# Performance work log

Measured on AMD Instinct MI355X. Metric: run time of the kernel, lower is better.

Reference implementation:

```python
import jax, jax.numpy as jnp
import numpy as np

B, C, E = 64, 32, 4
D_MODEL, PRED_LEN = 1024, 720
L_LIST = [32, 16, 8, 4]  # seq_len=512 / patch_sizes [16,32,64,128]
EPS = float(np.finfo(float).eps)


def setup_inputs() -> dict:
    key = jax.random.key(0)
    ks = jax.random.split(key, 16)
    inp = {}
    for i, L in enumerate(L_LIST):
        inp[f"xs{i}"] = jax.random.normal(ks[i], (B, C, L, D_MODEL), dtype=jnp.float32)
    inp["gates"] = jax.random.uniform(ks[4], (B, E), dtype=jnp.float32)
    w_scale = 1.0 / np.sqrt(D_MODEL)
    for i in range(E):
        inp[f"W{i}"] = jax.random.normal(ks[5 + i], (D_MODEL, PRED_LEN), dtype=jnp.float32) * w_scale
        inp[f"b{i}"] = jax.random.normal(ks[9 + i], (PRED_LEN,), dtype=jnp.float32) * 0.01
    return inp


def reference(xs0, xs1, xs2, xs3, gates, W0, b0, W1, b1, W2, b2, W3, b3):
    xs = [xs0, xs1, xs2, xs3]
    Ws = [W0, W1, W2, W3]
    bs = [b0, b1, b2, b3]
    # per-expert linear on last token: [B,C,D] @ [D,P] + [P] -> [B,C,P]
    outs = jnp.stack(
        [jnp.einsum("bcd,dp->bcp", x[:, :, -1, :], W) + b for x, W, b in zip(xs, Ws, bs)]
    )  # [E,B,C,P]
    # dense-gate combine(): sum_e gates[b,e] * exp(out_e[b])
    combined = jnp.einsum("ebcp,be->bcp", jnp.exp(outs), gates)  # [B,C,P]
    combined = jnp.where(combined == 0, EPS, combined)
    out = jnp.log(combined)  # [B,C,P]
    return out.transpose(0, 2, 1)  # 'B C P -> B P C'
```

## Files before the change

kernel.cpp:

```cpp
#include <hip/hip_runtime.h>
#include <hip/hip_bf16.h>


typedef __attribute__((ext_vector_type(4))) float f32x4;
typedef __attribute__((ext_vector_type(8))) short bf16x8;
typedef __attribute__((ext_vector_type(4))) unsigned short u16x4;
typedef __attribute__((ext_vector_type(8))) unsigned short u16x8;

#define EPSV 2.2204460492503131e-16f

__device__ __forceinline__ unsigned short f2bf(float f) {
  unsigned u = __builtin_bit_cast(unsigned, f);
  u += 0x7fffu + ((u >> 16) & 1u);
  return (unsigned short)(u >> 16);
}
__device__ __forceinline__ float bf2f(unsigned short h) {
  unsigned u = ((unsigned)h) << 16;
  return __builtin_bit_cast(float, u);
}

__device__ __forceinline__ void gload_lds16(const void* g, void* l) {
  __builtin_amdgcn_global_load_lds(
      (const __attribute__((address_space(1))) unsigned int*)g,
      (__attribute__((address_space(3))) unsigned int*)l, 16, 0, 0);
}

__global__ __launch_bounds__(256) void prep_fused(
    const float* __restrict__ xs0, const float* __restrict__ xs1,
    const float* __restrict__ xs2, const float* __restrict__ xs3,
    const float* __restrict__ W0, const float* __restrict__ W1,
    const float* __restrict__ W2, const float* __restrict__ W3,
    unsigned short* __restrict__ Xb, unsigned short* __restrict__ Wb)
{
  __shared__ __align__(16) unsigned short tile[64 * 72];
  const int tid = threadIdx.x;
  if (blockIdx.x < 4096) {
    const int i = blockIdx.x * 256 + tid;
    const int e = i >> 18;
    const int rem = i & 262143;
    const int m = rem >> 7;
    const int kc = rem & 127;
    const float* xp = (e == 0) ? xs0 : (e == 1) ? xs1 : (e == 2) ? xs2 : xs3;
    const int L = 32 >> e;
    const float* src = xp + ((size_t)m * L + (L - 1)) * 1024 + kc * 8;
    f32x4 v0 = *(const f32x4*)src;
    f32x4 v1 = *(const f32x4*)(src + 4);
    u16x8 pk;
    pk[0] = f2bf(v0[0]); pk[1] = f2bf(v0[1]); pk[2] = f2bf(v0[2]); pk[3] = f2bf(v0[3]);
    pk[4] = f2bf(v1[0]); pk[5] = f2bf(v1[1]); pk[6] = f2bf(v1[2]); pk[7] = f2bf(v1[3]);
    *(u16x8*)(Xb + ((size_t)e * 2048 + m) * 1024 + kc * 8) = pk;
  } else {
    const int wI = blockIdx.x - 4096;
    const int k0 = (wI & 15) * 64;
    const int rest = wI >> 4;
    const int nb = (rest % 12) * 64;
    const int e = rest / 12;
    const float* Wp = (e == 0) ? W0 : (e == 1) ? W1 : (e == 2) ? W2 : W3;
    const int n_c = tid & 15;
    const int r = tid >> 4;
    const int n0 = nb + n_c * 4;
#pragma unroll
    for (int j = 0; j < 4; ++j) {
      const int row = r + j * 16;
      f32x4 v = {0.f, 0.f, 0.f, 0.f};
      if (n0 < 720) v = *(const f32x4*)(Wp + (size_t)(k0 + row) * 720 + n0);
#pragma unroll
      for (int d = 0; d < 4; ++d) tile[(n_c * 4 + d) * 72 + row] = f2bf(v[d]);
    }
    __syncthreads();
    const int n_l = tid >> 2;
    const int kq = tid & 3;
    if (nb + n_l < 720) {
#pragma unroll
      for (int q = 0; q < 2; ++q) {
        const int chunk = q * 4 + kq;
        *(u16x8*)(Wb + ((size_t)e * 720 + nb + n_l) * 1024 + k0 + chunk * 8) =
            *(const u16x8*)(tile + n_l * 72 + chunk * 8);
      }
    }
  }
}

__global__ __launch_bounds__(256) void moe_gemm_e(
    const unsigned short* __restrict__ Xb, const unsigned short* __restrict__ Wb,
    const float* __restrict__ gates,
    const float* __restrict__ b0, const float* __restrict__ b1,
    const float* __restrict__ b2, const float* __restrict__ b3,
    unsigned short* __restrict__ planes)
{
  __shared__ __align__(16) unsigned char smem[49152];
  unsigned short* a_lds = (unsigned short*)smem;
  unsigned short* b_lds = (unsigned short*)(smem + 32768);

  const int tid = threadIdx.x;
  const int lane = tid & 63;
  const int wid = tid >> 6;
  const int wm = wid >> 1, wn = wid & 1;

  const int id = ((int)blockIdx.x & 7) * 96 + ((int)blockIdx.x >> 3);
  const int nt = id % 12;
  const int mt = (id / 12) % 16;
  const int e  = id / 192;
  const int nbase = nt * 64;

  const float* barr[4] = {b0, b1, b2, b3};
  float g_r[2];
#pragma unroll
  for (int h = 0; h < 2; ++h)
    g_r[h] = gates[(mt * 4 + wm * 2 + h) * 4 + e];
  float bias_r[2];
#pragma unroll
  for (int nf = 0; nf < 2; ++nf) {
    int col = nbase + wn * 32 + nf * 16 + (lane & 15);
    bias_r[nf] = barr[e][col < 720 ? col : 719];
  }

  const unsigned short* asrc = Xb + (size_t)e * 2048 * 1024 + (size_t)mt * 128 * 1024;
  const unsigned short* bsrc = Wb + (size_t)e * 720 * 1024;

  auto stage = [&](int k0, int buf) {
#pragma unroll
    for (int j = 0; j < 4; ++j) {
      const int C = j * 256 + tid;
      const int row = C >> 3, c = C & 7;
      gload_lds16(asrc + (size_t)row * 1024 + k0 + ((c ^ (row & 7)) * 8),
                  a_lds + buf * 8192 + C * 8);
    }
#pragma unroll
    for (int j = 0; j < 2; ++j) {
      const int C = j * 256 + tid;
      const int row = C >> 3, c = C & 7;
      int n = nbase + row; if (n > 719) n = 719;
      gload_lds16(bsrc + (size_t)n * 1024 + k0 + ((c ^ (row & 7)) * 8),
                  b_lds + buf * 4096 + C * 8);
    }
  };

  auto compute = [&](int buf, f32x4 (&acc)[4][2]) {
    const unsigned short* al = a_lds + buf * 8192;
    const unsigned short* bl = b_lds + buf * 4096;
#pragma unroll
    for (int ks = 0; ks < 2; ++ks) {
      const int kb = ks * 64 + (lane >> 4) * 16;
      bf16x8 af[4], bfm[2];
#pragma unroll
      for (int mf = 0; mf < 4; ++mf) {
        const int r = wm * 64 + mf * 16 + (lane & 15);
        const int byte = (r * 128 + kb) ^ ((r & 7) << 4);
        af[mf] = *(const bf16x8*)((const char*)al + byte);
      }
#pragma unroll
      for (int nf = 0; nf < 2; ++nf) {
        const int r = wn * 32 + nf * 16 + (lane & 15);
        const int byte = (r * 128 + kb) ^ ((r & 7) << 4);
        bfm[nf] = *(const bf16x8*)((const char*)bl + byte);
      }
#pragma unroll
      for (int mf = 0; mf < 4; ++mf)
#pragma unroll
        for (int nf = 0; nf < 2; ++nf)
          acc[mf][nf] = __builtin_amdgcn_mfma_f32_16x16x32_bf16(
              af[mf], bfm[nf], acc[mf][nf], 0, 0, 0);
    }
  };

  f32x4 acc[4][2] = {};
  int cur = 0;
  stage(0, 0);
  __syncthreads();
  for (int kt = 0; kt < 16; ++kt) {
    if (kt < 15) stage((kt + 1) * 64, cur ^ 1);
    compute(cur, acc);
    __syncthreads();
    cur ^= 1;
  }

#pragma unroll
  for (int nf = 0; nf < 2; ++nf) {
    const int p = nbase + wn * 32 + nf * 16 + (lane & 15);
    if (p < 720) {
#pragma unroll
      for (int mf = 0; mf < 4; ++mf) {
        const int m0 = mt * 128 + wm * 64 + mf * 16 + ((lane >> 4) << 2);
        const float g = g_r[mf >> 1];
        unsigned short* dst = planes + ((size_t)e * 2048 + m0) * 720 + p;
#pragma unroll
        for (int j = 0; j < 4; ++j)
          dst[j * 720] = f2bf(g * __expf(acc[mf][nf][j] + bias_r[nf]));
      }
    }
  }
}

__global__ __launch_bounds__(256) void reduce_log(
    const unsigned short* __restrict__ planes, float* __restrict__ out)
{
  __shared__ __align__(16) float t[64 * 36];
  const int nt = blockIdx.x;
  const int b  = blockIdx.y;
  const int nbase = nt * 64;
  const int tid = threadIdx.x;

  {
    const int row = tid >> 3;
    const int pc = tid & 7;
    int p0 = nbase + pc * 8;
    if (p0 > 712) p0 = 712;
    const size_t base = ((size_t)b * 32 + row) * 720 + p0;
    float s[8] = {};
#pragma unroll
    for (int pl = 0; pl < 4; ++pl) {
      u16x8 v = *(const u16x8*)(planes + (size_t)pl * 2048 * 720 + base);
#pragma unroll
      for (int d = 0; d < 8; ++d) s[d] += bf2f(v[d]);
    }
    const int pbase_l = (p0 - nbase);
#pragma unroll
    for (int d = 0; d < 8; ++d) {
      float v = s[d];
      v = (v == 0.0f) ? EPSV : v;
      t[(pbase_l + d) * 36 + row] = __logf(v);
    }
  }
  __syncthreads();
#pragma unroll
  for (int it = 0; it < 2; ++it) {
    const int i = it * 256 + tid;
    const int p_l = i >> 3;
    const int cc = i & 7;
    const int p = nbase + p_l;
    if (p < 720) {
      f32x4 v = *(const f32x4*)(t + p_l * 36 + cc * 4);
      *(f32x4*)(out + ((size_t)b * 720 + p) * 32 + cc * 4) = v;
    }
  }
}

__global__ __launch_bounds__(256) void moe_head_fallback(
    const float* __restrict__ xs0, const float* __restrict__ xs1,
    const float* __restrict__ xs2, const float* __restrict__ xs3,
    const float* __restrict__ gates,
    const float* __restrict__ W0, const float* __restrict__ b0,
    const float* __restrict__ W1, const float* __restrict__ b1,
    const float* __restrict__ W2, const float* __restrict__ b2,
    const float* __restrict__ W3, const float* __restrict__ b3,
    float* __restrict__ out)
{
  __shared__ __align__(16) unsigned short a_lds[64 * 64];
  __shared__ __align__(16) unsigned short b_lds[64 * 64];
  __shared__ __align__(16) float t_lds[4][32 * 36];
  const int tid = threadIdx.x;
  const int lane = tid & 63;
  const int wid = tid >> 6;
  const int wm = wid >> 1, wn = wid & 1;
  const int nt = blockIdx.x, mt = blockIdx.y;
  const int mbase = mt * 64, nbase = nt * 64;
  const float* xarr[4] = {xs0, xs1, xs2, xs3};
  const float* Warr[4] = {W0, W1, W2, W3};
  const float* barr[4] = {b0, b1, b2, b3};
  constexpr int Larr[4] = {32, 16, 8, 4};
  f32x4 comb[2][2] = {};
#pragma unroll
  for (int e = 0; e < 4; ++e) {
    const int L = Larr[e];
    const float* xlast = xarr[e] + (size_t)(L - 1) * 1024;
    const size_t xstride = (size_t)L * 1024;
    const float* Wp = Warr[e];
    f32x4 acc[2][2] = {};
    for (int kt = 0; kt < 16; ++kt) {
      const int k0 = kt * 64;
      __syncthreads();
      {
        const int k_l = (tid & 15) * 4;
        const int r0 = tid >> 4;
#pragma unroll
        for (int j = 0; j < 4; ++j) {
          const int row = r0 + j * 16;
          f32x4 v = *(const f32x4*)(xlast + (size_t)(mbase + row) * xstride + (k0 + k_l));
          u16x4 pk;
          pk[0] = f2bf(v[0]); pk[1] = f2bf(v[1]); pk[2] = f2bf(v[2]); pk[3] = f2bf(v[3]);
          const int byte = (row * 128 + k_l * 2) ^ ((row & 7) << 4);
          *(u16x4*)((char*)a_lds + byte) = pk;
        }
      }
      {
        const int n_l = tid & 63;
        const int kq = tid >> 6;
        const int n_g = nbase + n_l;
        const bool nok = (n_g < 720);
        const float* wcol = Wp + n_g;
#pragma unroll
        for (int g = 0; g < 4; ++g) {
          const int k_l = kq * 4 + g * 16;
          float w0 = 0.f, w1 = 0.f, w2 = 0.f, w3 = 0.f;
          if (nok) {
            const float* s = wcol + (size_t)(k0 + k_l) * 720;
            w0 = s[0]; w1 = s[720]; w2 = s[1440]; w3 = s[2160];
          }
          u16x4 pk;
          pk[0] = f2bf(w0); pk[1] = f2bf(w1); pk[2] = f2bf(w2); pk[3] = f2bf(w3);
          const int byte = (n_l * 128 + k_l * 2) ^ ((n_l & 7) << 4);
          *(u16x4*)((char*)b_lds + byte) = pk;
        }
      }
      __syncthreads();
#pragma unroll
      for (int ks = 0; ks < 2; ++ks) {
        const int kb2 = (ks * 32 + (lane >> 4) * 8) * 2;
        bf16x8 af[2], bfr[2];
#pragma unroll
        for (int mf = 0; mf < 2; ++mf) {
          const int r = wm * 32 + mf * 16 + (lane & 15);
          const int byte = (r * 128 + kb2) ^ ((r & 7) << 4);
          af[mf] = *(const bf16x8*)((const char*)a_lds + byte);
        }
#pragma unroll
        for (int nf = 0; nf < 2; ++nf) {
          const int r = wn * 32 + nf * 16 + (lane & 15);
          const int byte = (r * 128 + kb2) ^ ((r & 7) << 4);
          bfr[nf] = *(const bf16x8*)((const char*)b_lds + byte);
        }
#pragma unroll
        for (int mf = 0; mf < 2; ++mf)
#pragma unroll
          for (int nf = 0; nf < 2; ++nf)
            acc[mf][nf] = __builtin_amdgcn_mfma_f32_16x16x32_bf16(
                af[mf], bfr[nf], acc[mf][nf], 0, 0, 0);
      }
    }
    {
      const int b_idx = mt * 2 + wm;
      const float g = gates[b_idx * 4 + e];
#pragma unroll
      for (int nf = 0; nf < 2; ++nf) {
        const int col = nbase + wn * 32 + nf * 16 + (lane & 15);
        const float bias = (col < 720) ? barr[e][col] : 0.0f;
#pragma unroll
        for (int mf = 0; mf < 2; ++mf)
#pragma unroll
          for (int j = 0; j < 4; ++j)
            comb[mf][nf][j] += g * __expf(acc[mf][nf][j] + bias);
      }
    }
  }
  {
    float* tl = &t_lds[wid][0];
#pragma unroll
    for (int mf = 0; mf < 2; ++mf)
#pragma unroll
      for (int nf = 0; nf < 2; ++nf)
#pragma unroll
        for (int j = 0; j < 4; ++j) {
          const int row_l = mf * 16 + (lane >> 4) * 4 + j;
          const int col_l = nf * 16 + (lane & 15);
          float v = comb[mf][nf][j];
          v = (v == 0.0f) ? EPSV : v;
          tl[col_l * 36 + row_l] = __logf(v);
        }
    __syncthreads();
    const int b_idx = mt * 2 + wm;
    const int pbase = nbase + wn * 32;
#pragma unroll
    for (int it = 0; it < 4; ++it) {
      const int p_l = it * 8 + (lane >> 3);
      const int p = pbase + p_l;
      if (p < 720) {
        f32x4 v = *(const f32x4*)(tl + p_l * 36 + (lane & 7) * 4);
        *(f32x4*)(out + ((size_t)b_idx * 720 + p) * 32 + (lane & 7) * 4) = v;
      }
    }
  }
}

extern "C" void kernel_launch(void* const* d_in, const int* in_sizes, int n_in,
                              void* d_out, int out_size, void* d_ws, size_t ws_size,
                              hipStream_t stream) {
  const size_t xb_elems = (size_t)4 * 2048 * 1024;
  const size_t wb_elems = (size_t)4 * 720 * 1024;
  const size_t plane_elems = (size_t)4 * 2048 * 720;
  const size_t need = (xb_elems + wb_elems + plane_elems) * 2;
  if (ws_size >= need) {
    unsigned short* Xb = (unsigned short*)d_ws;
    unsigned short* Wb = Xb + xb_elems;
    unsigned short* planes = Wb + wb_elems;
    prep_fused<<<4096 + 768, 256, 0, stream>>>(
        (const float*)d_in[0], (const float*)d_in[1],
        (const float*)d_in[2], (const float*)d_in[3],
        (const float*)d_in[5], (const float*)d_in[7],
        (const float*)d_in[9], (const float*)d_in[11],
        Xb, Wb);
    moe_gemm_e<<<768, 256, 0, stream>>>(
        Xb, Wb, (const float*)d_in[4],
        (const float*)d_in[6], (const float*)d_in[8],
        (const float*)d_in[10], (const float*)d_in[12],
        planes);
    reduce_log<<<dim3(12, 64), 256, 0, stream>>>(planes, (float*)d_out);
  } else {
    moe_head_fallback<<<dim3(12, 32), 256, 0, stream>>>(
        (const float*)d_in[0], (const float*)d_in[1],
        (const float*)d_in[2], (const float*)d_in[3],
        (const float*)d_in[4],
        (const float*)d_in[5], (const float*)d_in[6],
        (const float*)d_in[7], (const float*)d_in[8],
        (const float*)d_in[9], (const float*)d_in[10],
        (const float*)d_in[11], (const float*)d_in[12],
        (float*)d_out);
  }
}
```

Before: 39.71 us.

## Pre-swizzle operands into MFMA fragment layout and load directly to registers

The prep kernel now writes X and W in bf16 laid out in the exact per-lane MFMA fragment order. The GEMM can then drop LDS staging, double buffering and barriers and read fragments straight from global memory with coalesced 16-byte loads. The GEMM block shrinks to 2 waves, each computing a 64x64 tile with a 4x4 accumulator grid. This removes LDS traffic and sync overhead, but gives up cross-wave reuse through shared memory. Each W fragment is now read from global or L2 by more waves, and memory latency is hidden only by occupancy and the 2x unroll.

After: 56.28 us. +41.7%, slower.

```diff
diff --git a/kernel.cpp b/kernel.cpp
--- a/kernel.cpp
+++ b/kernel.cpp
@@ -19,18 +19,13 @@
   return __builtin_bit_cast(float, u);
 }
 
-__device__ __forceinline__ void gload_lds16(const void* g, void* l) {
-  __builtin_amdgcn_global_load_lds(
-      (const __attribute__((address_space(1))) unsigned int*)g,
-      (__attribute__((address_space(3))) unsigned int*)l, 16, 0, 0);
-}
 
 __global__ __launch_bounds__(256) void prep_fused(
     const float* __restrict__ xs0, const float* __restrict__ xs1,
     const float* __restrict__ xs2, const float* __restrict__ xs3,
     const float* __restrict__ W0, const float* __restrict__ W1,
     const float* __restrict__ W2, const float* __restrict__ W3,
-    unsigned short* __restrict__ Xb, unsigned short* __restrict__ Wb)
+    unsigned short* __restrict__ Xf, unsigned short* __restrict__ Wf)
 {
   __shared__ __align__(16) unsigned short tile[64 * 72];
   const int tid = threadIdx.x;
@@ -48,7 +43,12 @@
     u16x8 pk;
     pk[0] = f2bf(v0[0]); pk[1] = f2bf(v0[1]); pk[2] = f2bf(v0[2]); pk[3] = f2bf(v0[3]);
     pk[4] = f2bf(v1[0]); pk[5] = f2bf(v1[1]); pk[6] = f2bf(v1[2]); pk[7] = f2bf(v1[3]);
-    *(u16x8*)(Xb + ((size_t)e * 2048 + m) * 1024 + kc * 8) = pk;
+    const int mp = m >> 6, mf = (m >> 4) & 3, ml = m & 15;
+    const int kt = kc >> 3, ks = (kc >> 2) & 1, kl = kc & 3;
+    const int lane = kl * 16 + ml;
+    const size_t dst = ((size_t)(((((e * 32 + mp) * 16 + kt) * 2 + ks) * 4 + mf)) * 512)
+                       + lane * 8;
+    *(u16x8*)(Xf + dst) = pk;
   } else {
     const int wI = blockIdx.x - 4096;
     const int k0 = (wI & 15) * 64;
@@ -70,123 +70,78 @@
     __syncthreads();
     const int n_l = tid >> 2;
     const int kq = tid & 3;
-    if (nb + n_l < 720) {
-#pragma unroll
-      for (int q = 0; q < 2; ++q) {
-        const int chunk = q * 4 + kq;
-        *(u16x8*)(Wb + ((size_t)e * 720 + nb + n_l) * 1024 + k0 + chunk * 8) =
-            *(const u16x8*)(tile + n_l * 72 + chunk * 8);
-      }
-    }
-  }
-}
-
-__global__ __launch_bounds__(256) void moe_gemm_e(
-    const unsigned short* __restrict__ Xb, const unsigned short* __restrict__ Wb,
+    const int np = nb >> 6;
+    const int kt = k0 >> 6;
+    const int nf = (n_l >> 4) & 3, nl = n_l & 15;
+#pragma unroll
+    for (int q = 0; q < 2; ++q) {
+      const int chunk = q * 4 + kq;
+      const int ks = chunk >> 2, kl = chunk & 3;
+      const size_t dst = ((size_t)(((((e * 12 + np) * 16 + kt) * 2 + ks) * 4 + nf)) * 512)
+                         + (kl * 16 + nl) * 8;
+      *(u16x8*)(Wf + dst) = *(const u16x8*)(tile + n_l * 72 + chunk * 8);
+    }
+  }
+}
+
+__global__ __launch_bounds__(128) void moe_gemm_frag(
+    const unsigned short* __restrict__ Xf, const unsigned short* __restrict__ Wf,
     const float* __restrict__ gates,
     const float* __restrict__ b0, const float* __restrict__ b1,
     const float* __restrict__ b2, const float* __restrict__ b3,
     unsigned short* __restrict__ planes)
 {
-  __shared__ __align__(16) unsigned char smem[49152];
-  unsigned short* a_lds = (unsigned short*)smem;
-  unsigned short* b_lds = (unsigned short*)(smem + 32768);
-
   const int tid = threadIdx.x;
   const int lane = tid & 63;
-  const int wid = tid >> 6;
-  const int wm = wid >> 1, wn = wid & 1;
+  const int wm = tid >> 6;
 
   const int id = ((int)blockIdx.x & 7) * 96 + ((int)blockIdx.x >> 3);
-  const int nt = id % 12;
-  const int mt = (id / 12) % 16;
-  const int e  = id / 192;
-  const int nbase = nt * 64;
+  const int np  = id % 12;
+  const int mtB = (id / 12) & 15;
+  const int e   = id / 192;
+  const int mp  = mtB * 2 + wm;
+
+  const unsigned short* A = Xf + (size_t)(e * 32 + mp) * 65536 + (size_t)lane * 8;
+  const unsigned short* B = Wf + (size_t)(e * 12 + np) * 65536 + (size_t)lane * 8;
+
+  f32x4 acc[4][4] = {};
+#pragma unroll 2
+  for (int kt = 0; kt < 16; ++kt) {
+#pragma unroll
+    for (int ks = 0; ks < 2; ++ks) {
+      const int off = kt * 4096 + ks * 2048;
+      bf16x8 af[4], bf[4];
+#pragma unroll
+      for (int mf = 0; mf < 4; ++mf) af[mf] = *(const bf16x8*)(A + off + mf * 512);
+#pragma unroll
+      for (int nf = 0; nf < 4; ++nf) bf[nf] = *(const bf16x8*)(B + off + nf * 512);
+#pragma unroll
+      for (int mf = 0; mf < 4; ++mf)
+#pragma unroll
+        for (int nf = 0; nf < 4; ++nf)
+          acc[mf][nf] = __builtin_amdgcn_mfma_f32_16x16x32_bf16(
+              af[mf], bf[nf], acc[mf][nf], 0, 0, 0);
+    }
+  }
 
   const float* barr[4] = {b0, b1, b2, b3};
   float g_r[2];
 #pragma unroll
   for (int h = 0; h < 2; ++h)
-    g_r[h] = gates[(mt * 4 + wm * 2 + h) * 4 + e];
-  float bias_r[2];
-#pragma unroll
-  for (int nf = 0; nf < 2; ++nf) {
-    int col = nbase + wn * 32 + nf * 16 + (lane & 15);
-    bias_r[nf] = barr[e][col < 720 ? col : 719];
-  }
-
-  const unsigned short* asrc = Xb + (size_t)e * 2048 * 1024 + (size_t)mt * 128 * 1024;
-  const unsigned short* bsrc = Wb + (size_t)e * 720 * 1024;
-
-  auto stage = [&](int k0, int buf) {
-#pragma unroll
-    for (int j = 0; j < 4; ++j) {
-      const int C = j * 256 + tid;
-      const int row = C >> 3, c = C & 7;
-      gload_lds16(asrc + (size_t)row * 1024 + k0 + ((c ^ (row & 7)) * 8),
-                  a_lds + buf * 8192 + C * 8);
-    }
-#pragma unroll
-    for (int j = 0; j < 2; ++j) {
-      const int C = j * 256 + tid;
-      const int row = C >> 3, c = C & 7;
-      int n = nbase + row; if (n > 719) n = 719;
-      gload_lds16(bsrc + (size_t)n * 1024 + k0 + ((c ^ (row & 7)) * 8),
-                  b_lds + buf * 4096 + C * 8);
-    }
-  };
-
-  auto compute = [&](int buf, f32x4 (&acc)[4][2]) {
-    const unsigned short* al = a_lds + buf * 8192;
-    const unsigned short* bl = b_lds + buf * 4096;
-#pragma unroll
-    for (int ks = 0; ks < 2; ++ks) {
-      const int kb = ks * 64 + (lane >> 4) * 16;
-      bf16x8 af[4], bfm[2];
+    g_r[h] = gates[(mp * 2 + h) * 4 + e];
+#pragma unroll
+  for (int nf = 0; nf < 4; ++nf) {
+    const int p = np * 64 + nf * 16 + (lane & 15);
+    if (p < 720) {
+      const float bias = barr[e][p];
 #pragma unroll
       for (int mf = 0; mf < 4; ++mf) {
-        const int r = wm * 64 + mf * 16 + (lane & 15);
-        const int byte = (r * 128 + kb) ^ ((r & 7) << 4);
-        af[mf] = *(const bf16x8*)((const char*)al + byte);
-      }
-#pragma unroll
-      for (int nf = 0; nf < 2; ++nf) {
-        const int r = wn * 32 + nf * 16 + (lane & 15);
-        const int byte = (r * 128 + kb) ^ ((r & 7) << 4);
-        bfm[nf] = *(const bf16x8*)((const char*)bl + byte);
-      }
-#pragma unroll
-      for (int mf = 0; mf < 4; ++mf)
-#pragma unroll
-        for (int nf = 0; nf < 2; ++nf)
-          acc[mf][nf] = __builtin_amdgcn_mfma_f32_16x16x32_bf16(
-              af[mf], bfm[nf], acc[mf][nf], 0, 0, 0);
-    }
-  };
-
-  f32x4 acc[4][2] = {};
-  int cur = 0;
-  stage(0, 0);
-  __syncthreads();
-  for (int kt = 0; kt < 16; ++kt) {
-    if (kt < 15) stage((kt + 1) * 64, cur ^ 1);
-    compute(cur, acc);
-    __syncthreads();
-    cur ^= 1;
-  }
-
-#pragma unroll
-  for (int nf = 0; nf < 2; ++nf) {
-    const int p = nbase + wn * 32 + nf * 16 + (lane & 15);
-    if (p < 720) {
-#pragma unroll
-      for (int mf = 0; mf < 4; ++mf) {
-        const int m0 = mt * 128 + wm * 64 + mf * 16 + ((lane >> 4) << 2);
+        const int m0 = mp * 64 + mf * 16 + ((lane >> 4) << 2);
+        unsigned short* dst = planes + ((size_t)e * 2048 + m0) * 720 + p;
         const float g = g_r[mf >> 1];
-        unsigned short* dst = planes + ((size_t)e * 2048 + m0) * 720 + p;
 #pragma unroll
         for (int j = 0; j < 4; ++j)
-          dst[j * 720] = f2bf(g * __expf(acc[mf][nf][j] + bias_r[nf]));
+          dst[j * 720] = f2bf(g * __expf(acc[mf][nf][j] + bias));
       }
     }
   }
@@ -375,22 +330,22 @@
 extern "C" void kernel_launch(void* const* d_in, const int* in_sizes, int n_in,
                               void* d_out, int out_size, void* d_ws, size_t ws_size,
                               hipStream_t stream) {
-  const size_t xb_elems = (size_t)4 * 2048 * 1024;
-  const size_t wb_elems = (size_t)4 * 720 * 1024;
+  const size_t xf_elems = (size_t)4 * 32 * 65536;
+  const size_t wf_elems = (size_t)4 * 12 * 65536;
   const size_t plane_elems = (size_t)4 * 2048 * 720;
-  const size_t need = (xb_elems + wb_elems + plane_elems) * 2;
+  const size_t need = (xf_elems + wf_elems + plane_elems) * 2;
   if (ws_size >= need) {
-    unsigned short* Xb = (unsigned short*)d_ws;
-    unsigned short* Wb = Xb + xb_elems;
-    unsigned short* planes = Wb + wb_elems;
+    unsigned short* Xf = (unsigned short*)d_ws;
+    unsigned short* Wf = Xf + xf_elems;
+    unsigned short* planes = Wf + wf_elems;
     prep_fused<<<4096 + 768, 256, 0, stream>>>(
         (const float*)d_in[0], (const float*)d_in[1],
         (const float*)d_in[2], (const float*)d_in[3],
         (const float*)d_in[5], (const float*)d_in[7],
         (const float*)d_in[9], (const float*)d_in[11],
-        Xb, Wb);
-    moe_gemm_e<<<768, 256, 0, stream>>>(
-        Xb, Wb, (const float*)d_in[4],
+        Xf, Wf);
+    moe_gemm_frag<<<768, 128, 0, stream>>>(
+        Xf, Wf, (const float*)d_in[4],
         (const float*)d_in[6], (const float*)d_in[8],
         (const float*)d_in[10], (const float*)d_in[12],
         planes);
```

## Fuse activation fp32-to-bf16 conversion into GEMM A-operand staging

Applied to the files above, without the earlier changes.

Removes the separate X conversion pass that wrote a bf16 copy of the last-token activations to workspace. The GEMM now loads fp32 activations directly from the strided inputs into registers, converts them to bf16 and writes them into swizzled LDS, prefetching one k-tile ahead. This drops a global write and re-read of the X buffer, but each k-step gains an extra barrier, and each block converts the A data again for every one of the 12 N-tiles.

New measurement: 44.29 us. 11.5% more time.

```diff
diff --git a/kernel.cpp b/kernel.cpp
--- a/kernel.cpp
+++ b/kernel.cpp
@@ -25,64 +25,47 @@
       (__attribute__((address_space(3))) unsigned int*)l, 16, 0, 0);
 }
 
-__global__ __launch_bounds__(256) void prep_fused(
+__global__ __launch_bounds__(256) void prep_w(
+    const float* __restrict__ W0, const float* __restrict__ W1,
+    const float* __restrict__ W2, const float* __restrict__ W3,
+    unsigned short* __restrict__ Wb)
+{
+  __shared__ __align__(16) unsigned short tile[64 * 72];
+  const int wI = blockIdx.x;
+  const int k0 = (wI & 15) * 64;
+  const int rest = wI >> 4;
+  const int nb = (rest % 12) * 64;
+  const int e = rest / 12;
+  const float* Wp = (e == 0) ? W0 : (e == 1) ? W1 : (e == 2) ? W2 : W3;
+  const int tid = threadIdx.x;
+  const int n_c = tid & 15;
+  const int r = tid >> 4;
+  const int n0 = nb + n_c * 4;
+#pragma unroll
+  for (int j = 0; j < 4; ++j) {
+    const int row = r + j * 16;
+    f32x4 v = {0.f, 0.f, 0.f, 0.f};
+    if (n0 < 720) v = *(const f32x4*)(Wp + (size_t)(k0 + row) * 720 + n0);
+#pragma unroll
+    for (int d = 0; d < 4; ++d) tile[(n_c * 4 + d) * 72 + row] = f2bf(v[d]);
+  }
+  __syncthreads();
+  const int n_l = tid >> 2;
+  const int kq = tid & 3;
+  if (nb + n_l < 720) {
+#pragma unroll
+    for (int q = 0; q < 2; ++q) {
+      const int chunk = q * 4 + kq;
+      *(u16x8*)(Wb + ((size_t)e * 720 + nb + n_l) * 1024 + k0 + chunk * 8) =
+          *(const u16x8*)(tile + n_l * 72 + chunk * 8);
+    }
+  }
+}
+
+__global__ __launch_bounds__(256) void moe_gemm_fx(
     const float* __restrict__ xs0, const float* __restrict__ xs1,
     const float* __restrict__ xs2, const float* __restrict__ xs3,
-    const float* __restrict__ W0, const float* __restrict__ W1,
-    const float* __restrict__ W2, const float* __restrict__ W3,
-    unsigned short* __restrict__ Xb, unsigned short* __restrict__ Wb)
-{
-  __shared__ __align__(16) unsigned short tile[64 * 72];
-  const int tid = threadIdx.x;
-  if (blockIdx.x < 4096) {
-    const int i = blockIdx.x * 256 + tid;
-    const int e = i >> 18;
-    const int rem = i & 262143;
-    const int m = rem >> 7;
-    const int kc = rem & 127;
-    const float* xp = (e == 0) ? xs0 : (e == 1) ? xs1 : (e == 2) ? xs2 : xs3;
-    const int L = 32 >> e;
-    const float* src = xp + ((size_t)m * L + (L - 1)) * 1024 + kc * 8;
-    f32x4 v0 = *(const f32x4*)src;
-    f32x4 v1 = *(const f32x4*)(src + 4);
-    u16x8 pk;
-    pk[0] = f2bf(v0[0]); pk[1] = f2bf(v0[1]); pk[2] = f2bf(v0[2]); pk[3] = f2bf(v0[3]);
-    pk[4] = f2bf(v1[0]); pk[5] = f2bf(v1[1]); pk[6] = f2bf(v1[2]); pk[7] = f2bf(v1[3]);
-    *(u16x8*)(Xb + ((size_t)e * 2048 + m) * 1024 + kc * 8) = pk;
-  } else {
-    const int wI = blockIdx.x - 4096;
-    const int k0 = (wI & 15) * 64;
-    const int rest = wI >> 4;
-    const int nb = (rest % 12) * 64;
-    const int e = rest / 12;
-    const float* Wp = (e == 0) ? W0 : (e == 1) ? W1 : (e == 2) ? W2 : W3;
-    const int n_c = tid & 15;
-    const int r = tid >> 4;
-    const int n0 = nb + n_c * 4;
-#pragma unroll
-    for (int j = 0; j < 4; ++j) {
-      const int row = r + j * 16;
-      f32x4 v = {0.f, 0.f, 0.f, 0.f};
-      if (n0 < 720) v = *(const f32x4*)(Wp + (size_t)(k0 + row) * 720 + n0);
-#pragma unroll
-      for (int d = 0; d < 4; ++d) tile[(n_c * 4 + d) * 72 + row] = f2bf(v[d]);
-    }
-    __syncthreads();
-    const int n_l = tid >> 2;
-    const int kq = tid & 3;
-    if (nb + n_l < 720) {
-#pragma unroll
-      for (int q = 0; q < 2; ++q) {
-        const int chunk = q * 4 + kq;
-        *(u16x8*)(Wb + ((size_t)e * 720 + nb + n_l) * 1024 + k0 + chunk * 8) =
-            *(const u16x8*)(tile + n_l * 72 + chunk * 8);
-      }
-    }
-  }
-}
-
-__global__ __launch_bounds__(256) void moe_gemm_e(
-    const unsigned short* __restrict__ Xb, const unsigned short* __restrict__ Wb,
+    const unsigned short* __restrict__ Wb,
     const float* __restrict__ gates,
     const float* __restrict__ b0, const float* __restrict__ b1,
     const float* __restrict__ b2, const float* __restrict__ b3,
@@ -103,6 +86,20 @@
   const int e  = id / 192;
   const int nbase = nt * 64;
 
+  const float* xp = (e == 0) ? xs0 : (e == 1) ? xs1 : (e == 2) ? xs2 : xs3;
+  const int L = 32 >> e;
+  const size_t xstride = (size_t)L * 1024;
+  const float* xbase = xp + (size_t)(L - 1) * 1024;
+
+  const int c8 = tid & 7;
+  const int r0 = tid >> 3;
+  const float* arow[4];
+#pragma unroll
+  for (int p = 0; p < 4; ++p)
+    arow[p] = xbase + (size_t)(mt * 128 + p * 32 + r0) * xstride + c8 * 8;
+
+  const unsigned short* bsrc = Wb + (size_t)e * 720 * 1024;
+
   const float* barr[4] = {b0, b1, b2, b3};
   float g_r[2];
 #pragma unroll
@@ -115,17 +112,27 @@
     bias_r[nf] = barr[e][col < 720 ? col : 719];
   }
 
-  const unsigned short* asrc = Xb + (size_t)e * 2048 * 1024 + (size_t)mt * 128 * 1024;
-  const unsigned short* bsrc = Wb + (size_t)e * 720 * 1024;
-
-  auto stage = [&](int k0, int buf) {
-#pragma unroll
-    for (int j = 0; j < 4; ++j) {
-      const int C = j * 256 + tid;
-      const int row = C >> 3, c = C & 7;
-      gload_lds16(asrc + (size_t)row * 1024 + k0 + ((c ^ (row & 7)) * 8),
-                  a_lds + buf * 8192 + C * 8);
-    }
+  f32x4 av[4][2];
+  auto ldA = [&](int k0) {
+#pragma unroll
+    for (int p = 0; p < 4; ++p) {
+      av[p][0] = *(const f32x4*)(arow[p] + k0);
+      av[p][1] = *(const f32x4*)(arow[p] + k0 + 4);
+    }
+  };
+  auto wrA = [&](int buf) {
+    char* ab = (char*)(a_lds + buf * 8192);
+#pragma unroll
+    for (int p = 0; p < 4; ++p) {
+      u16x8 pk;
+#pragma unroll
+      for (int d = 0; d < 4; ++d) { pk[d] = f2bf(av[p][0][d]); pk[d + 4] = f2bf(av[p][1][d]); }
+      const int r = p * 32 + r0;
+      const int byte = (r * 128 + c8 * 16) ^ ((r & 7) << 4);
+      *(u16x8*)(ab + byte) = pk;
+    }
+  };
+  auto stageW = [&](int k0, int buf) {
 #pragma unroll
     for (int j = 0; j < 2; ++j) {
       const int C = j * 256 + tid;
@@ -164,14 +171,25 @@
     }
   };
 
+  ldA(0);
+  stageW(0, 0);
+  wrA(0);
+  __syncthreads();
+
   f32x4 acc[4][2] = {};
   int cur = 0;
-  stage(0, 0);
-  __syncthreads();
   for (int kt = 0; kt < 16; ++kt) {
-    if (kt < 15) stage((kt + 1) * 64, cur ^ 1);
+    const bool hn = (kt < 15);
+    if (hn) {
+      ldA((kt + 1) * 64);
+      stageW((kt + 1) * 64, cur ^ 1);
+    }
     compute(cur, acc);
     __syncthreads();
+    if (hn) {
+      wrA(cur ^ 1);
+      __syncthreads();
+    }
     cur ^= 1;
   }
 
@@ -375,22 +393,19 @@
 extern "C" void kernel_launch(void* const* d_in, const int* in_sizes, int n_in,
                               void* d_out, int out_size, void* d_ws, size_t ws_size,
                               hipStream_t stream) {
-  const size_t xb_elems = (size_t)4 * 2048 * 1024;
   const size_t wb_elems = (size_t)4 * 720 * 1024;
   const size_t plane_elems = (size_t)4 * 2048 * 720;
-  const size_t need = (xb_elems + wb_elems + plane_elems) * 2;
+  const size_t need = (wb_elems + plane_elems) * 2;
   if (ws_size >= need) {
-    unsigned short* Xb = (unsigned short*)d_ws;
-    unsigned short* Wb = Xb + xb_elems;
+    unsigned short* Wb = (unsigned short*)d_ws;
     unsigned short* planes = Wb + wb_elems;
-    prep_fused<<<4096 + 768, 256, 0, stream>>>(
+    prep_w<<<768, 256, 0, stream>>>(
+        (const float*)d_in[5], (const float*)d_in[7],
+        (const float*)d_in[9], (const float*)d_in[11], Wb);
+    moe_gemm_fx<<<768, 256, 0, stream>>>(
         (const float*)d_in[0], (const float*)d_in[1],
         (const float*)d_in[2], (const float*)d_in[3],
-        (const float*)d_in[5], (const float*)d_in[7],
-        (const float*)d_in[9], (const float*)d_in[11],
-        Xb, Wb);
-    moe_gemm_e<<<768, 256, 0, stream>>>(
-        Xb, Wb, (const float*)d_in[4],
+        Wb, (const float*)d_in[4],
         (const float*)d_in[6], (const float*)d_in[8],
         (const float*)d_in[10], (const float*)d_in[12],
         planes);
```
